# Kernel optimization log

Hardware: AMD Instinct MI355X
Metric: run time of the kernel (lower is better)

## Reference

```python
import jax, jax.numpy as jnp
import numpy as np

B, Q, D = 4, 8, 128  # batch of volumes, poses per volume, volume side (L == D)


def setup_inputs() -> dict:
    key = jax.random.key(0)
    k1, k2 = jax.random.split(key)
    density = jax.random.normal(k1, (B, D, D, D), dtype=jnp.float32)
    rotation = jax.random.normal(k2, (B, Q, 3, 3), dtype=jnp.float32)
    return {"density": density, "rotation": rotation}


def _project(density, rotation):
    """density: (B, NZ, NY, NX); rotation: (B, Q, 3, 3) -> (B, Q, NY, NX).

    Replicates: rotate an L^3 coord grid, F.grid_sample (trilinear,
    align_corners=True, zero padding), then sum over the last grid axis.
    """
    b, NZ, NY, NX = density.shape
    q = rotation.shape[1]
    L = NZ  # module asserts D == NZ == NY == NX and uses L == D

    lin = jnp.linspace(-1.0, 1.0, L, dtype=density.dtype)
    xx, yy, zz = jnp.meshgrid(lin, lin, lin, indexing="ij")
    coords = jnp.stack([xx, yy, zz], axis=-1)  # (L, L, L, 3)

    Rf = rotation.reshape(b * q, 3, 3)
    # rot_coords[n,i,j,k,m] = sum_c coords[i,j,k,c] * R[n,c,m]
    rc = jnp.einsum("ijkc,ncm->nijkm", coords, Rf)  # (BQ, L, L, L, 3)

    # grid_sample convention: last dim is (x, y, z) indexing (NX, NY, NZ).
    # align_corners=True unnormalization: idx = (c + 1) / 2 * (size - 1)
    x = (rc[..., 0] + 1.0) * 0.5 * (NX - 1)
    y = (rc[..., 1] + 1.0) * 0.5 * (NY - 1)
    z = (rc[..., 2] + 1.0) * 0.5 * (NZ - 1)

    x0 = jnp.floor(x).astype(jnp.int32)
    y0 = jnp.floor(y).astype(jnp.int32)
    z0 = jnp.floor(z).astype(jnp.int32)
    fx = x - x0
    fy = y - y0
    fz = z - z0

    vol = jnp.broadcast_to(density[:, None], (b, q, NZ, NY, NX))
    vol_flat = vol.reshape(b * q, NZ * NY * NX)

    def corner(xc, yc, zc, w):
        valid = (xc >= 0) & (xc < NX) & (yc >= 0) & (yc < NY) & (zc >= 0) & (zc < NZ)
        xi = jnp.clip(xc, 0, NX - 1)
        yi = jnp.clip(yc, 0, NY - 1)
        zi = jnp.clip(zc, 0, NZ - 1)
        idx = (zi * NY + yi) * NX + xi  # (BQ, L, L, L)
        v = jnp.take_along_axis(vol_flat, idx.reshape(b * q, -1), axis=1)
        v = v.reshape(idx.shape)
        return jnp.where(valid, v, 0.0) * w

    sampled = (
        corner(x0,     y0,     z0,     (1 - fx) * (1 - fy) * (1 - fz))
        + corner(x0 + 1, y0,     z0,     fx * (1 - fy) * (1 - fz))
        + corner(x0,     y0 + 1, z0,     (1 - fx) * fy * (1 - fz))
        + corner(x0 + 1, y0 + 1, z0,     fx * fy * (1 - fz))
        + corner(x0,     y0,     z0 + 1, (1 - fx) * (1 - fy) * fz)
        + corner(x0 + 1, y0,     z0 + 1, fx * (1 - fy) * fz)
        + corner(x0,     y0 + 1, z0 + 1, (1 - fx) * fy * fz)
        + corner(x0 + 1, y0 + 1, z0 + 1, fx * fy * fz)
    )  # (BQ, L, L, L) over grid axes (X, Y, Z)

    sampled = sampled.reshape(b, q, L, L, L)
    proj = jnp.sum(sampled.transpose(0, 1, 3, 2, 4), axis=-1)  # (B, Q, L, L)
    return proj


def reference(density, rotation):
    return _project(density, rotation)
```

## Files before the change

### kernel.cpp

```cpp
#include <hip/hip_runtime.h>


#define LSZ 128
#define PACKED_BYTES ((size_t)4 * 128 * 128 * 128 * 8)

typedef float f2 __attribute__((ext_vector_type(2), aligned(4)));
typedef unsigned int u4v __attribute__((ext_vector_type(4), aligned(8)));

__device__ __forceinline__ float bl(unsigned int d) {
    return __uint_as_float(d << 16);
}
__device__ __forceinline__ float bh(unsigned int d) {
    return __uint_as_float(d & 0xffff0000u);
}

__device__ __forceinline__ unsigned int pk2(float lo, float hi) {
    unsigned int ul = __float_as_uint(lo), uh = __float_as_uint(hi);
    ul = (ul + 0x7fffu + ((ul >> 16) & 1u)) >> 16;
    uh = (uh + 0x7fffu + ((uh >> 16) & 1u)) >> 16;
    return ul | (uh << 16);
}

__global__ __launch_bounds__(128) void pack_kernel(
    const float* __restrict__ density, uint2* __restrict__ packed)
{
    const int x = threadIdx.x;
    const int y = blockIdx.x & 127;
    const int z = (blockIdx.x >> 7) & 127;
    const int b = blockIdx.x >> 14;
    const float* __restrict__ v = density + ((size_t)b << 21);
    const int y1 = min(y + 1, 127), z1 = min(z + 1, 127);
    const float vz0y0 = v[(z  << 14) + (y  << 7) + x];
    const float vz0y1 = v[(z  << 14) + (y1 << 7) + x];
    const float vz1y0 = v[(z1 << 14) + (y  << 7) + x];
    const float vz1y1 = v[(z1 << 14) + (y1 << 7) + x];
    packed[((size_t)b << 21) + (z << 14) + (y << 7) + x] =
        make_uint2(pk2(vz0y0, vz0y1), pk2(vz1y0, vz1y1));
}

#define PREP(S, kk) do {                                                      \
    const float kf_ = (float)(kk);                                            \
    const float X_ = fmaf(kf_, R20, Ax);                                      \
    const float Y_ = fmaf(kf_, R21, Ay);                                      \
    const float Z_ = fmaf(kf_, R22, Az);                                      \
    const int ix_ = (int)floorf(X_);                                          \
    const int iy_ = (int)floorf(Y_);                                          \
    const int iz_ = (int)floorf(Z_);                                          \
    const int ex_ = min(max(ix_, 0), 126);                                    \
    const int ey_ = min(max(iy_, 0), 126);                                    \
    const int ez_ = min(max(iz_, 0), 126);                                    \
    u##S = *(const u4v*)(vol2 + ((ez_ << 14) + (ey_ << 7) + ex_));            \
} while (0)

#define CONSUME(S, kk) do {                                                   \
    const float kf_ = (float)(kk);                                            \
    const float X_ = fmaf(kf_, R20, Ax);                                      \
    const float Y_ = fmaf(kf_, R21, Ay);                                      \
    const float Z_ = fmaf(kf_, R22, Az);                                      \
    const float xf_ = floorf(X_), yf_ = floorf(Y_), zf_ = floorf(Z_);         \
    const int ix_ = (int)xf_, iy_ = (int)yf_, iz_ = (int)zf_;                 \
    const float fx_ = X_ - xf_, fy_ = Y_ - yf_, fz_ = Z_ - zf_;               \
    const bool vx0_ = (ix_ >= 0)  & (ix_ <= 127);                             \
    const bool vx1_ = (ix_ >= -1) & (ix_ <= 126);                             \
    const bool vy0_ = (iy_ >= 0)  & (iy_ <= 127);                             \
    const bool vy1_ = (iy_ >= -1) & (iy_ <= 126);                             \
    const bool vz0_ = (iz_ >= 0)  & (iz_ <= 127);                             \
    const bool vz1_ = (iz_ >= -1) & (iz_ <= 126);                             \
    const float gx0 = vx0_ ? (1.0f - fx_) : 0.0f;                             \
    const float gx1 = vx1_ ? fx_ : 0.0f;                                      \
    const float gy0 = vy0_ ? (1.0f - fy_) : 0.0f;                             \
    const float gy1 = vy1_ ? fy_ : 0.0f;                                      \
    const float gz0 = vz0_ ? (1.0f - fz_) : 0.0f;                             \
    const float gz1 = vz1_ ? fz_ : 0.0f;                                      \
    const bool xhi_ = (ix_ > 126), xlo_ = (ix_ < 0);                          \
    const bool yhi_ = (iy_ > 126), ylo_ = (iy_ < 0);                          \
    const bool zhi_ = (iz_ > 126), zlo_ = (iz_ < 0);                          \
    const unsigned int a0z0 = xhi_ ? u##S.z : u##S.x;                         \
    const unsigned int a0z1 = xhi_ ? u##S.w : u##S.y;                         \
    const unsigned int a1z0 = xlo_ ? u##S.x : u##S.z;                         \
    const unsigned int a1z1 = xlo_ ? u##S.y : u##S.w;                         \
    const unsigned int dA = zhi_ ? a0z1 : a0z0;          \
    const unsigned int dB = zlo_ ? a0z0 : a0z1;          \
    const unsigned int dC = zhi_ ? a1z1 : a1z0;          \
    const unsigned int dD = zlo_ ? a1z0 : a1z1;          \
    const float c000 = yhi_ ? bh(dA) : bl(dA);                                \
    const float c010 = ylo_ ? bl(dA) : bh(dA);                                \
    const float c100 = yhi_ ? bh(dC) : bl(dC);                                \
    const float c110 = ylo_ ? bl(dC) : bh(dC);                                \
    const float c001 = yhi_ ? bh(dB) : bl(dB);                                \
    const float c011 = ylo_ ? bl(dB) : bh(dB);                                \
    const float c101 = yhi_ ? bh(dD) : bl(dD);                                \
    const float c111 = ylo_ ? bl(dD) : bh(dD);                                \
    const float s0_ = gy0 * fmaf(gx0, c000, gx1 * c100)                       \
                    + gy1 * fmaf(gx0, c010, gx1 * c110);                      \
    const float s1_ = gy0 * fmaf(gx0, c001, gx1 * c101)                       \
                    + gy1 * fmaf(gx0, c011, gx1 * c111);                      \
    acc = fmaf(gz0, s0_, fmaf(gz1, s1_, acc));                                \
} while (0)

__global__ __launch_bounds__(256) void proj_kernel_packed(
    const uint2* __restrict__ packed,
    const float* __restrict__ rotation,
    float* __restrict__ out)
{
    const int xcd  = blockIdx.x & 7;
    const int slot = blockIdx.x >> 3;
    const int b    = xcd >> 1;
    const int tile = ((xcd & 1) << 8) + slot;
    const int q    = tile >> 6;
    const int blk  = tile & 63;
    const int bq   = (b << 3) + q;

    const int p = (blk << 8) + threadIdx.x;
    const int i = p & (LSZ - 1);
    const int j = p >> 7;

    const float* R = rotation + bq * 9;
    const float R00 = R[0], R01 = R[1], R02 = R[2];
    const float R10 = R[3], R11 = R[4], R12 = R[5];
    const float R20 = R[6], R21 = R[7], R22 = R[8];

    const float step = 2.0f / 127.0f;
    const float li = -1.0f + (float)i * step;
    const float lj = -1.0f + (float)j * step;

    const float Ax = 63.5f * (li * R00 + lj * R10 - R20 + 1.0f);
    const float Ay = 63.5f * (li * R01 + lj * R11 - R21 + 1.0f);
    const float Az = 63.5f * (li * R02 + lj * R12 - R22 + 1.0f);

    float klo = 0.0f, khi = 127.0f;
    bool empty = false;
    {
        const float a[3] = {Ax, Ay, Az};
        const float s[3] = {R20, R21, R22};
        #pragma unroll
        for (int m = 0; m < 3; ++m) {
            if (fabsf(s[m]) > 1e-6f) {
                const float t0 = (-1.0f  - a[m]) / s[m];
                const float t1 = (128.0f - a[m]) / s[m];
                klo = fmaxf(klo, fminf(t0, t1));
                khi = fminf(khi, fmaxf(t0, t1));
            } else if (a[m] <= -1.0f || a[m] >= 128.0f) {
                empty = true;
            }
        }
    }
    int k_start = (int)ceilf(klo - 1e-3f);
    int k_end   = (int)floorf(khi + 1e-3f);
    if (k_start < 0) k_start = 0;
    if (k_end > 127) k_end = 127;
    if (empty) k_end = k_start - 1;

    const uint2* __restrict__ vol2 = packed + ((size_t)b << 21);

    float acc = 0.0f;
    u4v uA, uB, uC, uD;

    int n = k_end - k_start + 1;
    int k = k_start;
    if (n > 0) {
        PREP(A, k); PREP(B, k + 1); PREP(C, k + 2);
        while (n > 0) {
            PREP(D, k + 3);
            CONSUME(A, k);
            PREP(A, k + 4);
            if (n > 1) CONSUME(B, k + 1);
            PREP(B, k + 5);
            if (n > 2) CONSUME(C, k + 2);
            PREP(C, k + 6);
            if (n > 3) CONSUME(D, k + 3);
            k += 4; n -= 4;
        }
    }

    out[(bq << 14) + p] = acc;
}

#define FPREP(S, kk) do {                                                     \
    const float kf_ = (float)(kk);                                            \
    const float X_ = fmaf(kf_, R20, Ax);                                      \
    const float Y_ = fmaf(kf_, R21, Ay);                                      \
    const float Z_ = fmaf(kf_, R22, Az);                                      \
    const float xf_ = floorf(X_), yf_ = floorf(Y_), zf_ = floorf(Z_);         \
    const int ix_ = (int)xf_, iy_ = (int)yf_, iz_ = (int)zf_;                 \
    const float fx_ = X_ - xf_, fy_ = Y_ - yf_, fz_ = Z_ - zf_;               \
    const bool vx0_ = (ix_ >= 0)  & (ix_ <= 127);                             \
    const bool vx1_ = (ix_ >= -1) & (ix_ <= 126);                             \
    const bool vy0_ = (iy_ >= 0)  & (iy_ <= 127);                             \
    const bool vy1_ = (iy_ >= -1) & (iy_ <= 126);                             \
    const bool vz0_ = (iz_ >= 0)  & (iz_ <= 127);                             \
    const bool vz1_ = (iz_ >= -1) & (iz_ <= 126);                             \
    const int ex_  = min(max(ix_, 0), 126);                                   \
    s##S##hi = (ix_ > 126);                                                   \
    s##S##lo = (ix_ < 0);                                                     \
    const int cy0_ = min(max(iy_, 0), 127);                                   \
    const int cy1_ = min(max(iy_ + 1, 0), 127);                               \
    const int cz0_ = min(max(iz_, 0), 127);                                   \
    const int cz1_ = min(max(iz_ + 1, 0), 127);                               \
    g##S##x0 = vx0_ ? (1.0f - fx_) : 0.0f;                                    \
    g##S##x1 = vx1_ ? fx_ : 0.0f;                                             \
    g##S##y0 = vy0_ ? (1.0f - fy_) : 0.0f;                                    \
    g##S##y1 = vy1_ ? fy_ : 0.0f;                                             \
    g##S##z0 = vz0_ ? (1.0f - fz_) : 0.0f;                                    \
    g##S##z1 = vz1_ ? fz_ : 0.0f;                                             \
    const int z0o_ = cz0_ << 14, z1o_ = cz1_ << 14;                           \
    const int y0o_ = cy0_ << 7,  y1o_ = cy1_ << 7;                            \
    p##S##a = *(const f2*)(vol + (z0o_ + y0o_ + ex_));                        \
    p##S##b = *(const f2*)(vol + (z0o_ + y1o_ + ex_));                        \
    p##S##c = *(const f2*)(vol + (z1o_ + y0o_ + ex_));                        \
    p##S##d = *(const f2*)(vol + (z1o_ + y1o_ + ex_));                        \
} while (0)

#define FCONSUME(S) do {                                                      \
    const float c000 = s##S##hi ? p##S##a.y : p##S##a.x;                      \
    const float c100 = s##S##lo ? p##S##a.x : p##S##a.y;                      \
    const float c010 = s##S##hi ? p##S##b.y : p##S##b.x;                      \
    const float c110 = s##S##lo ? p##S##b.x : p##S##b.y;                      \
    const float c001 = s##S##hi ? p##S##c.y : p##S##c.x;                      \
    const float c101 = s##S##lo ? p##S##c.x : p##S##c.y;                      \
    const float c011 = s##S##hi ? p##S##d.y : p##S##d.x;                      \
    const float c111 = s##S##lo ? p##S##d.x : p##S##d.y;                      \
    const float s0_ = g##S##y0 * fmaf(g##S##x0, c000, g##S##x1 * c100)        \
                    + g##S##y1 * fmaf(g##S##x0, c010, g##S##x1 * c110);       \
    const float s1_ = g##S##y0 * fmaf(g##S##x0, c001, g##S##x1 * c101)        \
                    + g##S##y1 * fmaf(g##S##x0, c011, g##S##x1 * c111);       \
    acc = fmaf(g##S##z0, s0_, fmaf(g##S##z1, s1_, acc));                      \
} while (0)

__global__ __launch_bounds__(256) void proj_kernel_fallback(
    const float* __restrict__ density,
    const float* __restrict__ rotation,
    float* __restrict__ out)
{
    const int xcd  = blockIdx.x & 7;
    const int slot = blockIdx.x >> 3;
    const int b    = xcd >> 1;
    const int tile = ((xcd & 1) << 8) + slot;
    const int q    = tile >> 6;
    const int blk  = tile & 63;
    const int bq   = (b << 3) + q;

    const int p = (blk << 8) + threadIdx.x;
    const int i = p & (LSZ - 1);
    const int j = p >> 7;

    const float* R = rotation + bq * 9;
    const float R00 = R[0], R01 = R[1], R02 = R[2];
    const float R10 = R[3], R11 = R[4], R12 = R[5];
    const float R20 = R[6], R21 = R[7], R22 = R[8];

    const float step = 2.0f / 127.0f;
    const float li = -1.0f + (float)i * step;
    const float lj = -1.0f + (float)j * step;

    const float Ax = 63.5f * (li * R00 + lj * R10 - R20 + 1.0f);
    const float Ay = 63.5f * (li * R01 + lj * R11 - R21 + 1.0f);
    const float Az = 63.5f * (li * R02 + lj * R12 - R22 + 1.0f);

    float klo = 0.0f, khi = 127.0f;
    bool empty = false;
    {
        const float a[3] = {Ax, Ay, Az};
        const float s[3] = {R20, R21, R22};
        #pragma unroll
        for (int m = 0; m < 3; ++m) {
            if (fabsf(s[m]) > 1e-6f) {
                const float t0 = (-1.0f  - a[m]) / s[m];
                const float t1 = (128.0f - a[m]) / s[m];
                klo = fmaxf(klo, fminf(t0, t1));
                khi = fminf(khi, fmaxf(t0, t1));
            } else if (a[m] <= -1.0f || a[m] >= 128.0f) {
                empty = true;
            }
        }
    }
    int k_start = (int)ceilf(klo - 1e-3f);
    int k_end   = (int)floorf(khi + 1e-3f);
    if (k_start < 0) k_start = 0;
    if (k_end > 127) k_end = 127;
    if (empty) k_end = k_start - 1;

    const float* __restrict__ vol = density + (size_t)b * (LSZ * LSZ * LSZ);

    float acc = 0.0f;
    float gAx0, gAx1, gAy0, gAy1, gAz0, gAz1;
    f2 pAa, pAb, pAc, pAd;
    bool sAhi, sAlo;
    float gBx0, gBx1, gBy0, gBy1, gBz0, gBz1;
    f2 pBa, pBb, pBc, pBd;
    bool sBhi, sBlo;

    int k = k_start;
    if (k <= k_end) {
        FPREP(A, k);
        while (k <= k_end) {
            const int kn = k + 1;
            const bool hasB = (kn <= k_end);
            if (hasB) FPREP(B, kn);
            FCONSUME(A);
            if (hasB) FCONSUME(B);
            k += 2;
            if (k <= k_end) FPREP(A, k);
        }
    }

    out[(bq << 14) + p] = acc;
}

extern "C" void kernel_launch(void* const* d_in, const int* in_sizes, int n_in,
                              void* d_out, int out_size, void* d_ws, size_t ws_size,
                              hipStream_t stream) {
    const float* density  = (const float*)d_in[0];
    const float* rotation = (const float*)d_in[1];
    float* out = (float*)d_out;

    if (ws_size >= PACKED_BYTES) {
        uint2* packed = (uint2*)d_ws;
        pack_kernel<<<4 * 128 * 128, 128, 0, stream>>>(density, packed);
        proj_kernel_packed<<<2048, 256, 0, stream>>>(packed, rotation, out);
    } else {
        proj_kernel_fallback<<<2048, 256, 0, stream>>>(density, rotation, out);
    }
}
```

Measured before the change: 218.0 us.

## Split ray march into boundary-checked edges and branch-free interior segment

The projection loop is split into three k-ranges. The two edge ranges keep the full bounds-checked trilinear path. The interior range, where every corner is known to be in bounds, drops floor, clamps, validity masks and corner selects and uses truncation plus direct packed loads with a 4-deep prefetch. The pack kernel is also vectorised to float4 loads and uint4 stores with 256-thread blocks, and the fallback kernel is simplified to a plain loop. The margins chosen for the interior bounds (0.05, 126.95) carry some risk of edge-case errors if they are slightly off, and the extra loops add code size and register pressure.

```diff
diff --git a/kernel.cpp b/kernel.cpp
--- a/kernel.cpp
+++ b/kernel.cpp
@@ -13,7 +13,6 @@
 __device__ __forceinline__ float bh(unsigned int d) {
     return __uint_as_float(d & 0xffff0000u);
 }
-
 __device__ __forceinline__ unsigned int pk2(float lo, float hi) {
     unsigned int ul = __float_as_uint(lo), uh = __float_as_uint(hi);
     ul = (ul + 0x7fffu + ((ul >> 16) & 1u)) >> 16;
@@ -21,24 +20,59 @@
     return ul | (uh << 16);
 }
 
-__global__ __launch_bounds__(128) void pack_kernel(
+__global__ __launch_bounds__(256) void pack_kernel(
     const float* __restrict__ density, uint2* __restrict__ packed)
 {
-    const int x = threadIdx.x;
-    const int y = blockIdx.x & 127;
-    const int z = (blockIdx.x >> 7) & 127;
-    const int b = blockIdx.x >> 14;
+    const int t  = blockIdx.x * 256 + threadIdx.x;
+    const int xq = (t & 31) << 2;
+    const int y  = (t >> 5) & 127;
+    const int z  = (t >> 12) & 127;
+    const int b  = t >> 19;
     const float* __restrict__ v = density + ((size_t)b << 21);
     const int y1 = min(y + 1, 127), z1 = min(z + 1, 127);
-    const float vz0y0 = v[(z  << 14) + (y  << 7) + x];
-    const float vz0y1 = v[(z  << 14) + (y1 << 7) + x];
-    const float vz1y0 = v[(z1 << 14) + (y  << 7) + x];
-    const float vz1y1 = v[(z1 << 14) + (y1 << 7) + x];
-    packed[((size_t)b << 21) + (z << 14) + (y << 7) + x] =
-        make_uint2(pk2(vz0y0, vz0y1), pk2(vz1y0, vz1y1));
-}
-
-#define PREP(S, kk) do {                                                      \
+    const float4 a0 = *(const float4*)(v + (z  << 14) + (y  << 7) + xq);
+    const float4 a1 = *(const float4*)(v + (z  << 14) + (y1 << 7) + xq);
+    const float4 c0 = *(const float4*)(v + (z1 << 14) + (y  << 7) + xq);
+    const float4 c1 = *(const float4*)(v + (z1 << 14) + (y1 << 7) + xq);
+    uint4 o0, o1;
+    o0.x = pk2(a0.x, a1.x); o0.y = pk2(c0.x, c1.x);
+    o0.z = pk2(a0.y, a1.y); o0.w = pk2(c0.y, c1.y);
+    o1.x = pk2(a0.z, a1.z); o1.y = pk2(c0.z, c1.z);
+    o1.z = pk2(a0.w, a1.w); o1.w = pk2(c0.w, c1.w);
+    uint4* dst = (uint4*)(packed + ((size_t)b << 21) + (z << 14) + (y << 7) + xq);
+    dst[0] = o0; dst[1] = o1;
+}
+
+#define FPREPI(S, kk) do {                                                    \
+    const float kf_ = (float)min((kk), d);                                    \
+    const float X_ = fmaf(kf_, R20, Ax);                                      \
+    const float Y_ = fmaf(kf_, R21, Ay);                                      \
+    const float Z_ = fmaf(kf_, R22, Az);                                      \
+    const int ix_ = (int)X_;                                                  \
+    const int iy_ = (int)Y_;                                                  \
+    const int iz_ = (int)Z_;                                                  \
+    fx##S = X_ - (float)ix_;                                                  \
+    fy##S = Y_ - (float)iy_;                                                  \
+    fz##S = Z_ - (float)iz_;                                                  \
+    u##S = *(const u4v*)(vol2 + ((iz_ << 14) + (iy_ << 7) + ix_));            \
+} while (0)
+
+#define FCONSI(S) do {                                                        \
+    const float gx0 = 1.0f - fx##S;                                           \
+    const float gy0 = 1.0f - fy##S;                                           \
+    const float gz0 = 1.0f - fz##S;                                           \
+    const float c000 = bl(u##S.x), c010 = bh(u##S.x);                         \
+    const float c001 = bl(u##S.y), c011 = bh(u##S.y);                         \
+    const float c100 = bl(u##S.z), c110 = bh(u##S.z);                         \
+    const float c101 = bl(u##S.w), c111 = bh(u##S.w);                         \
+    const float s0_ = gy0   * fmaf(gx0, c000, fx##S * c100)                   \
+                    + fy##S * fmaf(gx0, c010, fx##S * c110);                  \
+    const float s1_ = gy0   * fmaf(gx0, c001, fx##S * c101)                   \
+                    + fy##S * fmaf(gx0, c011, fx##S * c111);                  \
+    acc = fmaf(gz0, s0_, fmaf(fz##S, s1_, acc));                              \
+} while (0)
+
+#define SPREP(S, kk) do {                                                     \
     const float kf_ = (float)(kk);                                            \
     const float X_ = fmaf(kf_, R20, Ax);                                      \
     const float Y_ = fmaf(kf_, R21, Ay);                                      \
@@ -52,7 +86,7 @@
     u##S = *(const u4v*)(vol2 + ((ez_ << 14) + (ey_ << 7) + ex_));            \
 } while (0)
 
-#define CONSUME(S, kk) do {                                                   \
+#define SCONS(S, kk) do {                                                     \
     const float kf_ = (float)(kk);                                            \
     const float X_ = fmaf(kf_, R20, Ax);                                      \
     const float Y_ = fmaf(kf_, R21, Ay);                                      \
@@ -79,10 +113,10 @@
     const unsigned int a0z1 = xhi_ ? u##S.w : u##S.y;                         \
     const unsigned int a1z0 = xlo_ ? u##S.x : u##S.z;                         \
     const unsigned int a1z1 = xlo_ ? u##S.y : u##S.w;                         \
-    const unsigned int dA = zhi_ ? a0z1 : a0z0;          \
-    const unsigned int dB = zlo_ ? a0z0 : a0z1;          \
-    const unsigned int dC = zhi_ ? a1z1 : a1z0;          \
-    const unsigned int dD = zlo_ ? a1z0 : a1z1;          \
+    const unsigned int dA = zhi_ ? a0z1 : a0z0;                               \
+    const unsigned int dB = zlo_ ? a0z0 : a0z1;                               \
+    const unsigned int dC = zhi_ ? a1z1 : a1z0;                               \
+    const unsigned int dD = zlo_ ? a1z0 : a1z1;                               \
     const float c000 = yhi_ ? bh(dA) : bl(dA);                                \
     const float c010 = ylo_ ? bl(dA) : bh(dA);                                \
     const float c100 = yhi_ ? bh(dC) : bl(dC);                                \
@@ -129,103 +163,102 @@
     const float Az = 63.5f * (li * R02 + lj * R12 - R22 + 1.0f);
 
     float klo = 0.0f, khi = 127.0f;
-    bool empty = false;
-    {
-        const float a[3] = {Ax, Ay, Az};
-        const float s[3] = {R20, R21, R22};
+    float klo2 = 0.0f, khi2 = 127.0f;
+    bool empty = false, empty2 = false;
+    {
+        const float a_[3] = {Ax, Ay, Az};
+        const float s_[3] = {R20, R21, R22};
         #pragma unroll
         for (int m = 0; m < 3; ++m) {
-            if (fabsf(s[m]) > 1e-6f) {
-                const float t0 = (-1.0f  - a[m]) / s[m];
-                const float t1 = (128.0f - a[m]) / s[m];
+            if (fabsf(s_[m]) > 1e-6f) {
+                const float r = 1.0f / s_[m];
+                const float t0 = (-1.0f   - a_[m]) * r;
+                const float t1 = (128.0f  - a_[m]) * r;
                 klo = fmaxf(klo, fminf(t0, t1));
                 khi = fminf(khi, fmaxf(t0, t1));
-            } else if (a[m] <= -1.0f || a[m] >= 128.0f) {
-                empty = true;
-            }
-        }
-    }
-    int k_start = (int)ceilf(klo - 1e-3f);
-    int k_end   = (int)floorf(khi + 1e-3f);
-    if (k_start < 0) k_start = 0;
-    if (k_end > 127) k_end = 127;
-    if (empty) k_end = k_start - 1;
+                const float w0 = (0.0f    - a_[m]) * r;
+                const float w1 = (126.95f - a_[m]) * r;
+                klo2 = fmaxf(klo2, fminf(w0, w1));
+                khi2 = fminf(khi2, fmaxf(w0, w1));
+            } else {
+                if (a_[m] <= -1.0f   || a_[m] >= 128.0f)   empty  = true;
+                if (a_[m] <  0.001f  || a_[m] >  126.94f)  empty2 = true;
+            }
+        }
+    }
+    int a = (int)ceilf(klo - 1e-3f);
+    int bnd = (int)floorf(khi + 1e-3f);
+    if (a < 0) a = 0;
+    if (bnd > 127) bnd = 127;
+    if (empty) bnd = a - 1;
+
+    int c = (int)ceilf(klo2 + 0.05f);
+    int d = (int)floorf(khi2 - 0.05f);
+    if (c < a) c = a;
+    if (d > bnd) d = bnd;
+    if (empty2 || d < c) { c = bnd + 1; d = bnd; }
 
     const uint2* __restrict__ vol2 = packed + ((size_t)b << 21);
 
     float acc = 0.0f;
     u4v uA, uB, uC, uD;
-
-    int n = k_end - k_start + 1;
-    int k = k_start;
-    if (n > 0) {
-        PREP(A, k); PREP(B, k + 1); PREP(C, k + 2);
-        while (n > 0) {
-            PREP(D, k + 3);
-            CONSUME(A, k);
-            PREP(A, k + 4);
-            if (n > 1) CONSUME(B, k + 1);
-            PREP(B, k + 5);
-            if (n > 2) CONSUME(C, k + 2);
-            PREP(C, k + 6);
-            if (n > 3) CONSUME(D, k + 3);
-            k += 4; n -= 4;
+    float fxA, fyA, fzA, fxB, fyB, fzB, fxC, fyC, fzC, fxD, fyD, fzD;
+
+    {
+        int k = a;
+        const int e = c - 1;
+        if (k <= e) {
+            SPREP(A, k);
+            while (k <= e) {
+                const int kn = k + 1;
+                const bool hasB = (kn <= e);
+                if (hasB) SPREP(B, kn);
+                SCONS(A, k);
+                if (hasB) SCONS(B, kn);
+                k += 2;
+                if (k <= e) SPREP(A, k);
+            }
+        }
+    }
+
+    {
+        int n = d - c + 1;
+        int k = c;
+        if (n > 0) {
+            FPREPI(A, k); FPREPI(B, k + 1); FPREPI(C, k + 2);
+            while (n > 0) {
+                FPREPI(D, k + 3);
+                FCONSI(A);
+                FPREPI(A, k + 4);
+                if (n > 1) FCONSI(B);
+                FPREPI(B, k + 5);
+                if (n > 2) FCONSI(C);
+                FPREPI(C, k + 6);
+                if (n > 3) FCONSI(D);
+                k += 4; n -= 4;
+            }
+        }
+    }
+
+    {
+        int k = d + 1;
+        const int e = bnd;
+        if (k <= e) {
+            SPREP(A, k);
+            while (k <= e) {
+                const int kn = k + 1;
+                const bool hasB = (kn <= e);
+                if (hasB) SPREP(B, kn);
+                SCONS(A, k);
+                if (hasB) SCONS(B, kn);
+                k += 2;
+                if (k <= e) SPREP(A, k);
+            }
         }
     }
 
     out[(bq << 14) + p] = acc;
 }
-
-#define FPREP(S, kk) do {                                                     \
-    const float kf_ = (float)(kk);                                            \
-    const float X_ = fmaf(kf_, R20, Ax);                                      \
-    const float Y_ = fmaf(kf_, R21, Ay);                                      \
-    const float Z_ = fmaf(kf_, R22, Az);                                      \
-    const float xf_ = floorf(X_), yf_ = floorf(Y_), zf_ = floorf(Z_);         \
-    const int ix_ = (int)xf_, iy_ = (int)yf_, iz_ = (int)zf_;                 \
-    const float fx_ = X_ - xf_, fy_ = Y_ - yf_, fz_ = Z_ - zf_;               \
-    const bool vx0_ = (ix_ >= 0)  & (ix_ <= 127);                             \
-    const bool vx1_ = (ix_ >= -1) & (ix_ <= 126);                             \
-    const bool vy0_ = (iy_ >= 0)  & (iy_ <= 127);                             \
-    const bool vy1_ = (iy_ >= -1) & (iy_ <= 126);                             \
-    const bool vz0_ = (iz_ >= 0)  & (iz_ <= 127);                             \
-    const bool vz1_ = (iz_ >= -1) & (iz_ <= 126);                             \
-    const int ex_  = min(max(ix_, 0), 126);                                   \
-    s##S##hi = (ix_ > 126);                                                   \
-    s##S##lo = (ix_ < 0);                                                     \
-    const int cy0_ = min(max(iy_, 0), 127);                                   \
-    const int cy1_ = min(max(iy_ + 1, 0), 127);                               \
-    const int cz0_ = min(max(iz_, 0), 127);                                   \
-    const int cz1_ = min(max(iz_ + 1, 0), 127);                               \
-    g##S##x0 = vx0_ ? (1.0f - fx_) : 0.0f;                                    \
-    g##S##x1 = vx1_ ? fx_ : 0.0f;                                             \
-    g##S##y0 = vy0_ ? (1.0f - fy_) : 0.0f;                                    \
-    g##S##y1 = vy1_ ? fy_ : 0.0f;                                             \
-    g##S##z0 = vz0_ ? (1.0f - fz_) : 0.0f;                                    \
-    g##S##z1 = vz1_ ? fz_ : 0.0f;                                             \
-    const int z0o_ = cz0_ << 14, z1o_ = cz1_ << 14;                           \
-    const int y0o_ = cy0_ << 7,  y1o_ = cy1_ << 7;                            \
-    p##S##a = *(const f2*)(vol + (z0o_ + y0o_ + ex_));                        \
-    p##S##b = *(const f2*)(vol + (z0o_ + y1o_ + ex_));                        \
-    p##S##c = *(const f2*)(vol + (z1o_ + y0o_ + ex_));                        \
-    p##S##d = *(const f2*)(vol + (z1o_ + y1o_ + ex_));                        \
-} while (0)
-
-#define FCONSUME(S) do {                                                      \
-    const float c000 = s##S##hi ? p##S##a.y : p##S##a.x;                      \
-    const float c100 = s##S##lo ? p##S##a.x : p##S##a.y;                      \
-    const float c010 = s##S##hi ? p##S##b.y : p##S##b.x;                      \
-    const float c110 = s##S##lo ? p##S##b.x : p##S##b.y;                      \
-    const float c001 = s##S##hi ? p##S##c.y : p##S##c.x;                      \
-    const float c101 = s##S##lo ? p##S##c.x : p##S##c.y;                      \
-    const float c011 = s##S##hi ? p##S##d.y : p##S##d.x;                      \
-    const float c111 = s##S##lo ? p##S##d.x : p##S##d.y;                      \
-    const float s0_ = g##S##y0 * fmaf(g##S##x0, c000, g##S##x1 * c100)        \
-                    + g##S##y1 * fmaf(g##S##x0, c010, g##S##x1 * c110);       \
-    const float s1_ = g##S##y0 * fmaf(g##S##x0, c001, g##S##x1 * c101)        \
-                    + g##S##y1 * fmaf(g##S##x0, c011, g##S##x1 * c111);       \
-    acc = fmaf(g##S##z0, s0_, fmaf(g##S##z1, s1_, acc));                      \
-} while (0)
 
 __global__ __launch_bounds__(256) void proj_kernel_fallback(
     const float* __restrict__ density,
@@ -260,16 +293,16 @@
     float klo = 0.0f, khi = 127.0f;
     bool empty = false;
     {
-        const float a[3] = {Ax, Ay, Az};
-        const float s[3] = {R20, R21, R22};
+        const float a_[3] = {Ax, Ay, Az};
+        const float s_[3] = {R20, R21, R22};
         #pragma unroll
         for (int m = 0; m < 3; ++m) {
-            if (fabsf(s[m]) > 1e-6f) {
-                const float t0 = (-1.0f  - a[m]) / s[m];
-                const float t1 = (128.0f - a[m]) / s[m];
+            if (fabsf(s_[m]) > 1e-6f) {
+                const float t0 = (-1.0f  - a_[m]) / s_[m];
+                const float t1 = (128.0f - a_[m]) / s_[m];
                 klo = fmaxf(klo, fminf(t0, t1));
                 khi = fminf(khi, fmaxf(t0, t1));
-            } else if (a[m] <= -1.0f || a[m] >= 128.0f) {
+            } else if (a_[m] <= -1.0f || a_[m] >= 128.0f) {
                 empty = true;
             }
         }
@@ -283,25 +316,47 @@
     const float* __restrict__ vol = density + (size_t)b * (LSZ * LSZ * LSZ);
 
     float acc = 0.0f;
-    float gAx0, gAx1, gAy0, gAy1, gAz0, gAz1;
-    f2 pAa, pAb, pAc, pAd;
-    bool sAhi, sAlo;
-    float gBx0, gBx1, gBy0, gBy1, gBz0, gBz1;
-    f2 pBa, pBb, pBc, pBd;
-    bool sBhi, sBlo;
-
-    int k = k_start;
-    if (k <= k_end) {
-        FPREP(A, k);
-        while (k <= k_end) {
-            const int kn = k + 1;
-            const bool hasB = (kn <= k_end);
-            if (hasB) FPREP(B, kn);
-            FCONSUME(A);
-            if (hasB) FCONSUME(B);
-            k += 2;
-            if (k <= k_end) FPREP(A, k);
-        }
+    for (int k = k_start; k <= k_end; ++k) {
+        const float kf = (float)k;
+        const float X = fmaf(kf, R20, Ax);
+        const float Y = fmaf(kf, R21, Ay);
+        const float Z = fmaf(kf, R22, Az);
+        const float xf = floorf(X), yf = floorf(Y), zf = floorf(Z);
+        const int ix = (int)xf, iy = (int)yf, iz = (int)zf;
+        const float fx = X - xf, fy = Y - yf, fz = Z - zf;
+        const bool vx0 = (ix >= 0)  & (ix <= 127);
+        const bool vx1 = (ix >= -1) & (ix <= 126);
+        const bool vy0 = (iy >= 0)  & (iy <= 127);
+        const bool vy1 = (iy >= -1) & (iy <= 126);
+        const bool vz0 = (iz >= 0)  & (iz <= 127);
+        const bool vz1 = (iz >= -1) & (iz <= 126);
+        const int cx0 = min(max(ix, 0), 127);
+        const int cx1 = min(max(ix + 1, 0), 127);
+        const int cy0 = min(max(iy, 0), 127);
+        const int cy1 = min(max(iy + 1, 0), 127);
+        const int cz0 = min(max(iz, 0), 127);
+        const int cz1 = min(max(iz + 1, 0), 127);
+        const float gx0 = vx0 ? (1.0f - fx) : 0.0f;
+        const float gx1 = vx1 ? fx : 0.0f;
+        const float gy0 = vy0 ? (1.0f - fy) : 0.0f;
+        const float gy1 = vy1 ? fy : 0.0f;
+        const float gz0 = vz0 ? (1.0f - fz) : 0.0f;
+        const float gz1 = vz1 ? fz : 0.0f;
+        const int z0o = cz0 << 14, z1o = cz1 << 14;
+        const int y0o = cy0 << 7,  y1o = cy1 << 7;
+        const float v000 = vol[z0o + y0o + cx0];
+        const float v100 = vol[z0o + y0o + cx1];
+        const float v010 = vol[z0o + y1o + cx0];
+        const float v110 = vol[z0o + y1o + cx1];
+        const float v001 = vol[z1o + y0o + cx0];
+        const float v101 = vol[z1o + y0o + cx1];
+        const float v011 = vol[z1o + y1o + cx0];
+        const float v111 = vol[z1o + y1o + cx1];
+        const float s0 = gy0 * fmaf(gx0, v000, gx1 * v100)
+                       + gy1 * fmaf(gx0, v010, gx1 * v110);
+        const float s1 = gy0 * fmaf(gx0, v001, gx1 * v101)
+                       + gy1 * fmaf(gx0, v011, gx1 * v111);
+        acc = fmaf(gz0, s0, fmaf(gz1, s1, acc));
     }
 
     out[(bq << 14) + p] = acc;
@@ -316,7 +371,7 @@
 
     if (ws_size >= PACKED_BYTES) {
         uint2* packed = (uint2*)d_ws;
-        pack_kernel<<<4 * 128 * 128, 128, 0, stream>>>(density, packed);
+        pack_kernel<<<8192, 256, 0, stream>>>(density, packed);
         proj_kernel_packed<<<2048, 256, 0, stream>>>(packed, rotation, out);
     } else {
         proj_kernel_fallback<<<2048, 256, 0, stream>>>(density, rotation, out);
```

Result: faster. 207.6 us (-4.8%).
